# Kernel optimization log

Measured on AMD Instinct MI355X. Metric: run time of the kernel, lower is better.

## Reference

```python
import jax, jax.numpy as jnp
import numpy as np

P = 1048576      # number of sampled ray points
H = 524288       # number of sparse voxels
NEMB = 600000    # number of corner embeddings (total_num_embedding)
D = 32           # voxel_embed_dim
VOXEL_SIZE = 0.25


def setup_inputs() -> dict:
    key = jax.random.key(0)
    k1, k2, k3, k4, k5 = jax.random.split(key, 5)
    point_xyz = jax.random.normal(k1, (H, 3), dtype=jnp.float32) * 5.0
    values = jax.random.normal(k2, (NEMB, D), dtype=jnp.float32)
    sampled_idx = jax.random.randint(k3, (P,), 0, H, dtype=jnp.int64)
    point_feats = jax.random.randint(k4, (H, 8), 0, NEMB, dtype=jnp.int64)
    # sample points lie inside their voxel (realistic, keeps interp weights in [0,1])
    jitter = (jax.random.uniform(k5, (P, 3), dtype=jnp.float32) - 0.5) * VOXEL_SIZE
    sampled_xyz = point_xyz[sampled_idx] + jitter
    return {
        "sampled_xyz": sampled_xyz,
        "point_xyz": point_xyz,
        "values": values,
        "sampled_idx": sampled_idx,
        "point_feats": point_feats,
    }


def _corner_q(dtype):
    # offset_points(p, 0.5, offset_only=True) + 0.5 -> {0,1}^3 corners, torch 'ij' meshgrid order
    c = jnp.arange(2)
    q = jnp.stack(jnp.meshgrid(c, c, c, indexing="ij"), axis=-1).reshape(8, 3)
    return q.astype(dtype)  # [8,3]


def reference(sampled_xyz, point_xyz, values, sampled_idx, point_feats):
    # gather per-sample voxel center and its 8 corner embedding ids
    pxyz = point_xyz[sampled_idx]        # [P,3]
    pf = point_feats[sampled_idx]        # [P,8]
    feats = values[pf]                   # [P,8,D]  (F.embedding)
    # normalized position inside voxel, in [0,1]^3
    p = (sampled_xyz - pxyz) / VOXEL_SIZE + 0.5   # [P,3]
    q = _corner_q(p.dtype)                        # [8,3]
    # trilinear weights: prod over xyz of (p*q + (1-p)*(1-q))
    w = jnp.prod(p[:, None, :] * q[None] + (1.0 - p[:, None, :]) * (1.0 - q[None]), axis=-1)  # [P,8]
    return jnp.einsum("pc,pcd->pd", w, feats)     # [P,D]
```

## Files before the change

### kernel.cpp

```cpp
#include <hip/hip_runtime.h>


#define VOXEL_INV 4.0f
#define CAP 8

typedef float vfloat4 __attribute__((ext_vector_type(4)));

__device__ __forceinline__ void corner_ids(const int* __restrict__ point_feats,
                                           int vi, int* ids)
{
    const int4* pf4 = (const int4*)(point_feats + ((size_t)vi << 3));
    int4 f0 = pf4[0];
    int4 f1 = pf4[1];
    ids[0] = f0.x; ids[1] = f0.y; ids[2] = f0.z; ids[3] = f0.w;
    ids[4] = f1.x; ids[5] = f1.y; ids[6] = f1.z; ids[7] = f1.w;
}

__device__ void compute_point_direct(
    const float* __restrict__ point_xyz,
    const float* __restrict__ values,
    const int*   __restrict__ point_feats,
    float*       __restrict__ out,
    int vi, int p, float sx, float sy, float sz)
{
    float cx = point_xyz[(size_t)vi * 3 + 0];
    float cy = point_xyz[(size_t)vi * 3 + 1];
    float cz = point_xyz[(size_t)vi * 3 + 2];

    float px = (sx - cx) * VOXEL_INV + 0.5f;
    float py = (sy - cy) * VOXEL_INV + 0.5f;
    float pz = (sz - cz) * VOXEL_INV + 0.5f;

    float xs[2] = {1.0f - px, px};
    float ys[2] = {1.0f - py, py};
    float zs[2] = {1.0f - pz, pz};

    int ids[8];
    corner_ids(point_feats, vi, ids);

    vfloat4 acc[8] = {};
#pragma unroll
    for (int c = 0; c < 8; ++c) {
        float w = xs[(c >> 2) & 1] * ys[(c >> 1) & 1] * zs[c & 1];
        const vfloat4* vr = (const vfloat4*)(values + ((size_t)ids[c] << 5));
#pragma unroll
        for (int k = 0; k < 8; ++k) acc[k] += w * vr[k];
    }
    vfloat4* o = (vfloat4*)(out + ((size_t)p << 5));
#pragma unroll
    for (int k = 0; k < 8; ++k) __builtin_nontemporal_store(acc[k], o + k);
}

__global__ __launch_bounds__(256) void svenc_direct(
    const float* __restrict__ sampled_xyz,
    const float* __restrict__ point_xyz,
    const float* __restrict__ values,
    const int*   __restrict__ sampled_idx,
    const int*   __restrict__ point_feats,
    float*       __restrict__ out,
    int P)
{
    int t   = blockIdx.x * blockDim.x + threadIdx.x;
    int pid = t >> 3;
    int sub = t & 7;
    if (pid >= P) return;

    int vi = __builtin_nontemporal_load(sampled_idx + pid);
    float sx = __builtin_nontemporal_load(sampled_xyz + pid * 3 + 0);
    float sy = __builtin_nontemporal_load(sampled_xyz + pid * 3 + 1);
    float sz = __builtin_nontemporal_load(sampled_xyz + pid * 3 + 2);

    float cx = point_xyz[(size_t)vi * 3 + 0];
    float cy = point_xyz[(size_t)vi * 3 + 1];
    float cz = point_xyz[(size_t)vi * 3 + 2];

    float px = (sx - cx) * VOXEL_INV + 0.5f;
    float py = (sy - cy) * VOXEL_INV + 0.5f;
    float pz = (sz - cz) * VOXEL_INV + 0.5f;

    float xs[2] = {1.0f - px, px};
    float ys[2] = {1.0f - py, py};
    float zs[2] = {1.0f - pz, pz};

    int ids[8];
    corner_ids(point_feats, vi, ids);

    vfloat4 acc = {0.0f, 0.0f, 0.0f, 0.0f};
#pragma unroll
    for (int c = 0; c < 8; ++c) {
        float w = xs[(c >> 2) & 1] * ys[(c >> 1) & 1] * zs[c & 1];
        const vfloat4 v = ((const vfloat4*)(values + ((size_t)ids[c] << 5)))[sub];
        acc += w * v;
    }
    __builtin_nontemporal_store(acc, (vfloat4*)(out + ((size_t)pid << 5)) + sub);
}

__global__ __launch_bounds__(256) void k_bucket_id(
    const float* __restrict__ sampled_xyz,
    const float* __restrict__ point_xyz,
    const float* __restrict__ values,
    const int*   __restrict__ sampled_idx,
    const int*   __restrict__ point_feats,
    float*       __restrict__ out,
    int*         __restrict__ counts,
    int*         __restrict__ bucket,
    int P)
{
    int p = blockIdx.x * 256 + threadIdx.x;
    if (p >= P) return;

    int vi = __builtin_nontemporal_load(sampled_idx + p);
    int pos = atomicAdd(counts + vi, 1);
    if (pos < CAP) {
        bucket[((size_t)vi << 3) + pos] = p;
    } else {
        float sx = sampled_xyz[(size_t)p * 3 + 0];
        float sy = sampled_xyz[(size_t)p * 3 + 1];
        float sz = sampled_xyz[(size_t)p * 3 + 2];
        compute_point_direct(point_xyz, values, point_feats, out, vi, p, sx, sy, sz);
    }
}

__global__ __launch_bounds__(256) void svenc_voxel_id(
    const float* __restrict__ sampled_xyz,
    const float* __restrict__ point_xyz,
    const float* __restrict__ values,
    const int*   __restrict__ point_feats,
    const int*   __restrict__ counts,
    const int*   __restrict__ bucket,
    float*       __restrict__ out,
    int H)
{
    int t   = blockIdx.x * 256 + threadIdx.x;
    int g   = t >> 3;
    int sub = t & 7;
    int lane = threadIdx.x & 63;
    if (g >= H) return;

    int n = counts[g];

    int myslot = bucket[((size_t)g << 3) + sub];

    if (n == 0) return;
    if (n > CAP) n = CAP;

    float cx = point_xyz[(size_t)g * 3 + 0];
    float cy = point_xyz[(size_t)g * 3 + 1];
    float cz = point_xyz[(size_t)g * 3 + 2];

    int ids[8];
    corner_ids(point_feats, g, ids);

    vfloat4 v[8];
#pragma unroll
    for (int c = 0; c < 8; ++c)
        v[c] = ((const vfloat4*)(values + ((size_t)ids[c] << 5)))[sub];

    int grpbase = lane & 56;
    for (int i = 0; i < n; ++i) {
        int p = __shfl(myslot, grpbase + i, 64);

        float sx = sampled_xyz[(size_t)p * 3 + 0];
        float sy = sampled_xyz[(size_t)p * 3 + 1];
        float sz = sampled_xyz[(size_t)p * 3 + 2];

        float px = (sx - cx) * VOXEL_INV + 0.5f;
        float py = (sy - cy) * VOXEL_INV + 0.5f;
        float pz = (sz - cz) * VOXEL_INV + 0.5f;

        float xs[2] = {1.0f - px, px};
        float ys[2] = {1.0f - py, py};
        float zs[2] = {1.0f - pz, pz};

        vfloat4 acc = {0.0f, 0.0f, 0.0f, 0.0f};
#pragma unroll
        for (int c = 0; c < 8; ++c) {
            float w = xs[(c >> 2) & 1] * ys[(c >> 1) & 1] * zs[c & 1];
            acc += w * v[c];
        }
        __builtin_nontemporal_store(acc, (vfloat4*)(out + ((size_t)p << 5)) + sub);
    }
}

extern "C" void kernel_launch(void* const* d_in, const int* in_sizes, int n_in,
                              void* d_out, int out_size, void* d_ws, size_t ws_size,
                              hipStream_t stream) {
    const float* sampled_xyz = (const float*)d_in[0];
    const float* point_xyz   = (const float*)d_in[1];
    const float* values      = (const float*)d_in[2];
    const int*   sampled_idx = (const int*)d_in[3];
    const int*   point_feats = (const int*)d_in[4];
    float* out = (float*)d_out;

    int P = in_sizes[3];

    int H;
    if (in_sizes[0] == 3 * P)       H = in_sizes[4] / 8;
    else                            H = in_sizes[4];

    size_t bucketB = (size_t)H * CAP * 4;
    size_t need    = bucketB + (size_t)H * 4;

    if (d_ws != nullptr && ws_size >= need && H > 0) {
        int* bucket = (int*)d_ws;
        int* counts = (int*)((char*)d_ws + bucketB);
        hipMemsetAsync(counts, 0, (size_t)H * 4, stream);

        int gp = (P + 255) / 256;
        k_bucket_id<<<gp, 256, 0, stream>>>(
            sampled_xyz, point_xyz, values, sampled_idx, point_feats,
            out, counts, bucket, P);

        long tt = (long)H * 8;
        int gm = (int)((tt + 255) / 256);
        svenc_voxel_id<<<gm, 256, 0, stream>>>(
            sampled_xyz, point_xyz, values, point_feats, counts, bucket, out, H);
    } else {
        long total_threads = (long)P * 8;
        int grid = (int)((total_threads + 255) / 256);
        svenc_direct<<<grid, 256, 0, stream>>>(
            sampled_xyz, point_xyz, values, sampled_idx, point_feats, out, P);
    }
}
```

Before: 372.1 us.

## Partition voxel bucket counters by block index to spread atomic contention

Replaces the single per-voxel counter with eight per-partition counters chosen by block index, each partition holding up to three slots in a 24-slot bucket. The consumer kernel reads its partition's count and slots per sub-lane, uses a ballot to skip empty voxels, and walks the partitions via shuffles. The aim is to cut atomic contention and serialisation on a shared counter. In exchange the memset grows eightfold, the bucket array triples, and more points may overflow a partition and take the slow direct path.

```diff
diff --git a/kernel.cpp b/kernel.cpp
--- a/kernel.cpp
+++ b/kernel.cpp
@@ -2,7 +2,9 @@
 
 
 #define VOXEL_INV 4.0f
-#define CAP 8
+#define NPART 8
+#define CAP_X 3
+#define SLOTS 24
 
 typedef float vfloat4 __attribute__((ext_vector_type(4)));
 
@@ -95,7 +97,7 @@
     __builtin_nontemporal_store(acc, (vfloat4*)(out + ((size_t)pid << 5)) + sub);
 }
 
-__global__ __launch_bounds__(256) void k_bucket_id(
+__global__ __launch_bounds__(256) void k_bucket_part(
     const float* __restrict__ sampled_xyz,
     const float* __restrict__ point_xyz,
     const float* __restrict__ values,
@@ -104,15 +106,17 @@
     float*       __restrict__ out,
     int*         __restrict__ counts,
     int*         __restrict__ bucket,
-    int P)
+    int P, int H)
 {
     int p = blockIdx.x * 256 + threadIdx.x;
     if (p >= P) return;
 
+    int x  = blockIdx.x & (NPART - 1);
     int vi = __builtin_nontemporal_load(sampled_idx + p);
-    int pos = atomicAdd(counts + vi, 1);
-    if (pos < CAP) {
-        bucket[((size_t)vi << 3) + pos] = p;
+
+    int pos = atomicAdd(counts + (size_t)x * H + vi, 1);
+    if (pos < CAP_X) {
+        bucket[(size_t)vi * SLOTS + x * CAP_X + pos] = p;
     } else {
         float sx = sampled_xyz[(size_t)p * 3 + 0];
         float sy = sampled_xyz[(size_t)p * 3 + 1];
@@ -121,7 +125,7 @@
     }
 }
 
-__global__ __launch_bounds__(256) void svenc_voxel_id(
+__global__ __launch_bounds__(256) void svenc_voxel_part(
     const float* __restrict__ sampled_xyz,
     const float* __restrict__ point_xyz,
     const float* __restrict__ values,
@@ -131,18 +135,20 @@
     float*       __restrict__ out,
     int H)
 {
-    int t   = blockIdx.x * 256 + threadIdx.x;
-    int g   = t >> 3;
-    int sub = t & 7;
+    int t    = blockIdx.x * 256 + threadIdx.x;
+    int g    = t >> 3;
+    int sub  = t & 7;
     int lane = threadIdx.x & 63;
+    int grpbase = lane & 56;
     if (g >= H) return;
 
-    int n = counts[g];
-
-    int myslot = bucket[((size_t)g << 3) + sub];
-
-    if (n == 0) return;
-    if (n > CAP) n = CAP;
+    int c = counts[(size_t)sub * H + g];
+    if (c > CAP_X) c = CAP_X;
+    const int* bs = bucket + (size_t)g * SLOTS + sub * CAP_X;
+    int s0 = bs[0], s1 = bs[1], s2 = bs[2];
+
+    unsigned long long any = __ballot(c > 0);
+    if (((any >> grpbase) & 0xFFull) == 0) return;
 
     float cx = point_xyz[(size_t)g * 3 + 0];
     float cy = point_xyz[(size_t)g * 3 + 1];
@@ -153,13 +159,10 @@
 
     vfloat4 v[8];
 #pragma unroll
-    for (int c = 0; c < 8; ++c)
-        v[c] = ((const vfloat4*)(values + ((size_t)ids[c] << 5)))[sub];
-
-    int grpbase = lane & 56;
-    for (int i = 0; i < n; ++i) {
-        int p = __shfl(myslot, grpbase + i, 64);
-
+    for (int cc = 0; cc < 8; ++cc)
+        v[cc] = ((const vfloat4*)(values + ((size_t)ids[cc] << 5)))[sub];
+
+    auto body = [&](int p) {
         float sx = sampled_xyz[(size_t)p * 3 + 0];
         float sy = sampled_xyz[(size_t)p * 3 + 1];
         float sz = sampled_xyz[(size_t)p * 3 + 2];
@@ -174,11 +177,20 @@
 
         vfloat4 acc = {0.0f, 0.0f, 0.0f, 0.0f};
 #pragma unroll
-        for (int c = 0; c < 8; ++c) {
-            float w = xs[(c >> 2) & 1] * ys[(c >> 1) & 1] * zs[c & 1];
-            acc += w * v[c];
+        for (int cc = 0; cc < 8; ++cc) {
+            float w = xs[(cc >> 2) & 1] * ys[(cc >> 1) & 1] * zs[cc & 1];
+            acc += w * v[cc];
         }
         __builtin_nontemporal_store(acc, (vfloat4*)(out + ((size_t)p << 5)) + sub);
+    };
+
+    for (int x = 0; x < NPART; ++x) {
+        int nx = __shfl(c, grpbase + x, 64);
+        if (nx == 0) continue;
+        int p0 = __shfl(s0, grpbase + x, 64);
+        body(p0);
+        if (nx > 1) { int p1 = __shfl(s1, grpbase + x, 64); body(p1); }
+        if (nx > 2) { int p2 = __shfl(s2, grpbase + x, 64); body(p2); }
     }
 }
 
@@ -198,22 +210,23 @@
     if (in_sizes[0] == 3 * P)       H = in_sizes[4] / 8;
     else                            H = in_sizes[4];
 
-    size_t bucketB = (size_t)H * CAP * 4;
-    size_t need    = bucketB + (size_t)H * 4;
+    size_t bucketB = (size_t)H * SLOTS * 4;
+    size_t countsB = (size_t)NPART * H * 4;
+    size_t need    = bucketB + countsB;
 
     if (d_ws != nullptr && ws_size >= need && H > 0) {
         int* bucket = (int*)d_ws;
         int* counts = (int*)((char*)d_ws + bucketB);
-        hipMemsetAsync(counts, 0, (size_t)H * 4, stream);
+        hipMemsetAsync(counts, 0, countsB, stream);
 
         int gp = (P + 255) / 256;
-        k_bucket_id<<<gp, 256, 0, stream>>>(
+        k_bucket_part<<<gp, 256, 0, stream>>>(
             sampled_xyz, point_xyz, values, sampled_idx, point_feats,
-            out, counts, bucket, P);
+            out, counts, bucket, P, H);
 
         long tt = (long)H * 8;
         int gm = (int)((tt + 255) / 256);
-        svenc_voxel_id<<<gm, 256, 0, stream>>>(
+        svenc_voxel_part<<<gm, 256, 0, stream>>>(
             sampled_xyz, point_xyz, values, point_feats, counts, bucket, out, H);
     } else {
         long total_threads = (long)P * 8;
```

After: 398.8 us. 7.2% more time.
